# Performance work log

Measured on AMD Instinct MI355X. Metric: run time of the kernel, lower is better.

## Reference

```python
import jax, jax.numpy as jnp
import numpy as np

B, T, V, E, H, L = 128, 512, 128, 256, 1024, 2


def setup_inputs() -> dict:
    key = jax.random.key(0)
    ks = jax.random.split(key, 8)
    scale_e = 1.0 / np.sqrt(E)
    scale0 = 1.0 / np.sqrt(E + H)
    scale1 = 1.0 / np.sqrt(2 * H)
    return {
        "input_batch": jax.random.randint(ks[0], (B, T), 0, V, dtype=jnp.int32),
        "input_lengths": jax.random.randint(ks[1], (B,), 1, T + 1, dtype=jnp.int32),
        "char_embeddings": jax.random.normal(ks[2], (V, E), dtype=jnp.float32) * scale_e,
        "W0": jax.random.normal(ks[3], (E + H, 4 * H), dtype=jnp.float32) * scale0,
        "b0": jnp.zeros((4 * H,), dtype=jnp.float32),
        "W1": jax.random.normal(ks[4], (2 * H, 4 * H), dtype=jnp.float32) * scale1,
        "b1": jnp.zeros((4 * H,), dtype=jnp.float32),
    }


def _lstm_cell(x, h, c, W, b):
    # TF BasicLSTMCell: gates in order (i, j, f, o), forget_bias = 1.0
    z = jnp.concatenate([x, h], axis=-1) @ W + b  # [B, 4H]
    i, j, f, o = jnp.split(z, 4, axis=-1)
    new_c = c * jax.nn.sigmoid(f + 1.0) + jax.nn.sigmoid(i) * jnp.tanh(j)
    new_h = jnp.tanh(new_c) * jax.nn.sigmoid(o)
    return new_h, new_c


def reference(input_batch, input_lengths, char_embeddings, W0, b0, W1, b1):
    # embedding lookup: [B, T, E] -> time-major [T, B, E]
    xs = jnp.swapaxes(char_embeddings[input_batch], 0, 1)
    t_idx = jnp.arange(T, dtype=jnp.int32)
    zeros = jnp.zeros((B, H), dtype=xs.dtype)
    init = (zeros, zeros, zeros, zeros)  # (h0, c0, h1, c1)

    def step(carry, inp):
        h0, c0, h1, c1 = carry
        x_t, t = inp
        mask = (t < input_lengths)[:, None]  # [B, 1] dynamic_rnn length mask
        nh0, nc0 = _lstm_cell(x_t, h0, c0, W0, b0)
        nh0 = jnp.where(mask, nh0, h0)
        nc0 = jnp.where(mask, nc0, c0)
        nh1, nc1 = _lstm_cell(nh0, h1, c1, W1, b1)
        nh1 = jnp.where(mask, nh1, h1)
        nc1 = jnp.where(mask, nc1, c1)
        out = jnp.where(mask, nh1, 0.0)  # dynamic_rnn zeros outputs past length
        return (nh0, nc0, nh1, nc1), out

    _, outputs = jax.lax.scan(step, init, (xs, t_idx))  # outputs: [T, B, H]
    outputs_bt = jnp.swapaxes(outputs, 0, 1)  # [B, T, H]
    # reverse_sequence + slice[:, 0, :] == output at last valid timestep
    idx = (input_lengths - 1)[:, None, None]  # [B, 1, 1]
    encoder_last_output = jnp.take_along_axis(outputs_bt, idx, axis=1)[:, 0, :]
    return encoder_last_output  # [B, H]
```

## Files before the change

### kernel.cpp

```cpp
#include <hip/hip_runtime.h>


namespace {
constexpr int NBLK = 256, THREADS = 512;
constexpr int KT0B = 40;
constexpr int KT1B = 64;
constexpr int NPH = 513;
constexpr int HPS = 128 * 1024;
constexpr int SPIN_CAP = 2000000;
constexpr int F_CREG  = 0;
constexpr int F_BOOT  = 128;
constexpr int F_GARR  = 256;
constexpr int F_XDONE = 768;
constexpr int F_XARR  = 1024;
}

typedef _Float16 f16x8 __attribute__((ext_vector_type(8)));
typedef float f32x4 __attribute__((ext_vector_type(4)));
typedef unsigned u32x4 __attribute__((ext_vector_type(4)));

__host__ __device__ __forceinline__ int fswz(int kk) {
  return ((kk & 15) >> 2) * 8 + (kk >> 4) * 4 + (kk & 3);
}

__device__ __forceinline__ float sigm(float x) { return 1.0f / (1.0f + __expf(-x)); }
__device__ __forceinline__ float tanh_f(float x) {
  float e = __expf(-2.0f * fabsf(x));
  float r = (1.0f - e) / (1.0f + e);
  return x >= 0.0f ? r : -r;
}
__device__ __forceinline__ unsigned short f2h(float f) {
  _Float16 h = (_Float16)f;
  return __builtin_bit_cast(unsigned short, h);
}

__device__ __forceinline__ int load_i32_llc(const int* p) {
  int v;
  asm volatile("global_load_dword %0, %1, off sc0 sc1\n\ts_waitcnt vmcnt(0)"
               : "=v"(v) : "v"(p) : "memory");
  return v;
}
__device__ __forceinline__ uint4 llc_load_issue(const unsigned* p) {
  uint4 v;
  asm volatile("global_load_dwordx4 %0, %1, off sc0 sc1" : "=v"(v) : "v"(p));
  return v;
}
__device__ __forceinline__ void vm_wait0() {
  asm volatile("s_waitcnt vmcnt(0)" ::: "memory");
  __builtin_amdgcn_sched_barrier(0);
}
__device__ __forceinline__ void store_u32_llc(unsigned* p, unsigned v) {
  asm volatile("global_store_dword %0, %1, off sc0 sc1" :: "v"(p), "v"(v) : "memory");
}
__device__ __forceinline__ void store_u16_llc(unsigned short* p, unsigned short v) {
  asm volatile("global_store_short %0, %1, off sc0 sc1" :: "v"(p), "v"(v) : "memory");
}
__device__ __forceinline__ void inv_l1() {
  asm volatile("buffer_inv" ::: "memory");
}
__device__ __forceinline__ int xcc_id() {
  int x;
  asm("s_getreg_b32 %0, hwreg(HW_REG_XCC_ID)" : "=s"(x));
  return x & 7;
}
__device__ __forceinline__ int spin_ge(int* p, int target) {
  for (int it = 0; it < SPIN_CAP; ++it) {
    if (load_i32_llc(p) >= target) return 1;
    __builtin_amdgcn_s_sleep(1);
  }
  return 0;
}
__device__ __forceinline__ f16x8 ash(u32x4 v) { return __builtin_bit_cast(f16x8, v); }
__device__ __forceinline__ f16x8 ash4(uint4 v) { return __builtin_bit_cast(f16x8, v); }

#define MFMA1(acc, ah, bh)                                                    \
  acc = __builtin_amdgcn_mfma_f32_16x16x32_f16(ah, bh, acc, 0, 0, 0);


__global__ void prep_sort(const int* __restrict__ lens, int* __restrict__ perm,
                          int* __restrict__ lenS, int* __restrict__ ncnt) {
  __shared__ int k_[128], p_[128];
  const int tid = threadIdx.x;
  if (tid < 128) { k_[tid] = (lens[tid] << 8) | (127 - tid); p_[tid] = tid; }
  __syncthreads();
  for (int ph = 0; ph < 128; ++ph) {
    if (tid < 64) {
      int a = 2 * tid + (ph & 1), b = a + 1;
      if (b < 128 && k_[a] < k_[b]) {
        int tk = k_[a]; k_[a] = k_[b]; k_[b] = tk;
        int tp = p_[a]; p_[a] = p_[b]; p_[b] = tp;
      }
    }
    __syncthreads();
  }
  if (tid < 128) { perm[tid] = p_[tid]; lenS[tid] = k_[tid] >> 8; }
  if (tid < 512) {
    int c = 0;
    for (int i = 0; i < 128; ++i) c += ((k_[i] >> 8) > tid) ? 1 : 0;
    ncnt[tid] = c;
  }
}

__global__ void prep_emb(const float* __restrict__ emb,
                         unsigned short* __restrict__ ef) {
  int i = blockIdx.x * 256 + threadIdx.x;
  int row = i >> 8, e = i & 255;
  int pos = row * 256 + (e >> 5) * 32 + fswz(e & 31);
  ef[pos] = f2h(emb[i]);
}

__global__ void prep_wslab(const float* __restrict__ W, uint4* __restrict__ Whi,
                           int KT) {
  int e = blockIdx.x * 256 + threadIdx.x;
  int lane = e & 63;
  int kt = (e >> 6) % KT;
  int blk = e / (64 * KT);
  int cf = lane & 15;
  int g = cf & 3, ul = cf >> 2;
  int col = g * 1024 + blk * 4 + ul;
  int kbase = kt * 32 + ((lane >> 4) & 3) * 4;
  unsigned hi[8];
#pragma unroll
  for (int j = 0; j < 8; ++j) {
    int k = kbase + (j & 3) + 16 * (j >> 2);
    float f = W[(size_t)k * 4096 + col];
    hi[j] = __builtin_bit_cast(unsigned short, (_Float16)f);
  }
  uint4 vh;
  vh.x = hi[0] | (hi[1] << 16); vh.y = hi[2] | (hi[3] << 16);
  vh.z = hi[4] | (hi[5] << 16); vh.w = hi[6] | (hi[7] << 16);
  Whi[e] = vh;
}


__global__ __launch_bounds__(THREADS, 1) void lstm_persist(
    const int* __restrict__ ib,
    const float* __restrict__ bias0, const float* __restrict__ bias1,
    const uint4* __restrict__ Whi0g, const uint4* __restrict__ Whi1g,
    const unsigned short* __restrict__ embF,
    const int* __restrict__ perm, const int* __restrict__ lenS,
    const int* __restrict__ ncnt,
    unsigned short* hg0, unsigned short* hg1,
    unsigned short* rep,
    int* ctr, float* __restrict__ out) {
  const int bid = blockIdx.x;
  const int tid = threadIdx.x;
  const int w = tid >> 6;
  const int lane = tid & 63;
  const int lr = lane & 15;
  const int lg4 = ((lane >> 4) & 3) * 4;
  const int slotE = ((lane >> 4) & 3) * 8;
  const int arow = w * 16 + lr;
  const int srow = tid >> 2;
  const int cu = tid & 3;
  const int ug = bid * 4 + cu;
  const int fpos = (ug >> 5) * 32 + fswz(ug & 31);
  const int permA = perm[arow];
  const int cperm = perm[srow];
  const int clen = lenS[srow];

  __shared__ uint4 Wh0[KT0B * 64];
  __shared__ uint4 Wh1[KT1B * 64];
  __shared__ float zb[2][128][17];
  __shared__ int s_x, s_rk, s_R, s_pres, s_ok;

  {
    const uint4* s0 = Whi0g + (size_t)bid * (KT0B * 64);
    for (int i = tid; i < KT0B * 64; i += THREADS) Wh0[i] = s0[i];
    const uint4* s1 = Whi1g + (size_t)bid * (KT1B * 64);
    for (int i = tid; i < KT1B * 64; i += THREADS) Wh1[i] = s1[i];
  }

  float bz0[4], bz1[4];
#pragma unroll
  for (int g = 0; g < 4; ++g) {
    bz0[g] = bias0[g * 1024 + ug];
    bz1[g] = bias1[g * 1024 + ug];
  }
  float c0r = 0.0f, c1r = 0.0f;

  if (tid == 0) {
    s_ok = 1;
    int x = xcc_id();
    s_x = x;
    s_rk = atomicAdd(&ctr[F_CREG + x * 16], 1);
    vm_wait0();
    atomicAdd(&ctr[F_BOOT], 1);
    if (!spin_ge(&ctr[F_BOOT], NBLK)) s_ok = 0;
    int Rv = 1, pres = 0;
    for (int i = 0; i < 8; ++i) {
      int r = load_i32_llc(&ctr[F_CREG + i * 16]);
      if (r > 0) pres |= (1 << i);
      if (i == s_x) Rv = r;
    }
    s_R = Rv;
    s_pres = pres;
  }
  __syncthreads();
  const int xcd = s_x, rk = s_rk, R = s_R, pres = s_pres;
  if (!s_ok) return;

  unsigned short* repB = rep + (size_t)xcd * 2 * HPS;
  const unsigned short* A0 = repB + (size_t)arow * 1024;
  const unsigned short* A1 = repB + HPS + (size_t)arow * 1024;

  const int pl = tid >> 8;
  const int rowoff = (tid >> 7) & 1;
  const int ch = (tid & 127) * 8;
  unsigned short* dp = repB + pl * HPS;

  f32x4 acc0 = (f32x4){0.f, 0.f, 0.f, 0.f};
  if (w * 16 < ncnt[0]) {
    const unsigned short* ef = embF + ib[(size_t)permA * 512] * 256;
#pragma unroll
    for (int kt = 0; kt < 8; ++kt) {
      const f16x8 ah = ash(*(const u32x4*)(ef + kt * 32 + slotE));
      MFMA1(acc0, ah, ash4(Wh0[kt * 64 + lane]))
    }
  }

  for (int p = 0; p < NPH; ++p) {
    const int nact0 = (p < 512) ? ncnt[p] : 0;
    const int nact1 = (p >= 1) ? ncnt[p - 1] : 0;
    const bool doL0 = (p < 512) && (w * 16 < nact0);
    const bool doL1 = (p >= 1) && (w * 16 < nact1);
    const int ncopy = ncnt[p == 0 ? 0 : p - 1];

    f32x4 acc1 = (f32x4){0.f, 0.f, 0.f, 0.f};

    {
      const unsigned short* sp =
          (pl == 0) ? (hg0 + (size_t)((p + 2) % 3) * HPS)
                    : (hg1 + (size_t)((p + 1) % 3) * HPS);
      const int step = 2 * R;
      const int dr0 = 2 * rk + rowoff;
      const int dr1 = dr0 + step, dr2 = dr0 + 2 * step, dr3 = dr0 + 3 * step;
      uint4 dv0, dv1, dv2, dv3;
      if (dr0 < ncopy) dv0 = llc_load_issue((const unsigned*)(sp + dr0 * 1024 + ch));
      if (dr1 < ncopy) dv1 = llc_load_issue((const unsigned*)(sp + dr1 * 1024 + ch));
      if (dr2 < ncopy) dv2 = llc_load_issue((const unsigned*)(sp + dr2 * 1024 + ch));
      if (dr3 < ncopy) dv3 = llc_load_issue((const unsigned*)(sp + dr3 * 1024 + ch));
      vm_wait0();
      if (dr0 < ncopy) *(uint4*)(dp + dr0 * 1024 + ch) = dv0;
      if (dr1 < ncopy) *(uint4*)(dp + dr1 * 1024 + ch) = dv1;
      if (dr2 < ncopy) *(uint4*)(dp + dr2 * 1024 + ch) = dv2;
      if (dr3 < ncopy) *(uint4*)(dp + dr3 * 1024 + ch) = dv3;
      for (int r = dr0 + 4 * step; r < ncopy; r += step) {
        uint4 v = llc_load_issue((const unsigned*)(sp + r * 1024 + ch));
        vm_wait0();
        *(uint4*)(dp + r * 1024 + ch) = v;
      }
    }
    __syncthreads();

    if (tid == 0) store_u32_llc((unsigned*)&ctr[F_XARR + xcd * 64 + rk], p + 1);
    if (tid < 64 && tid < R) {
      if (!spin_ge(&ctr[F_XARR + xcd * 64 + tid], p + 1)) s_ok = 0;
    }
    __syncthreads();
    if (!s_ok) break;
    inv_l1();

    if (doL0 || doL1) {
      u32x4 a[2][8];
#pragma unroll
      for (int i = 0; i < 8; ++i) a[0][i] = *(const u32x4*)(A0 + i * 32 + slotE);
#pragma unroll
      for (int g = 0; g < 4; ++g) {
        const int cb = g & 1;
        if (g < 3) {
#pragma unroll
          for (int i = 0; i < 8; ++i)
            a[cb ^ 1][i] = *(const u32x4*)(A0 + ((g + 1) * 8 + i) * 32 + slotE);
        } else if (doL1) {
#pragma unroll
          for (int i = 0; i < 8; ++i)
            a[cb ^ 1][i] = *(const u32x4*)(A1 + i * 32 + slotE);
        }
#pragma unroll
        for (int i = 0; i < 8; ++i) {
          const int q = g * 8 + i;
          const f16x8 ah = ash(a[cb][i]);
          if (doL0) { MFMA1(acc0, ah, ash4(Wh0[(8 + q) * 64 + lane])) }
          if (doL1) { MFMA1(acc1, ah, ash4(Wh1[q * 64 + lane])) }
        }
      }
      if (doL1) {
#pragma unroll
        for (int g = 0; g < 4; ++g) {
          const int cb = g & 1;
          if (g < 3) {
#pragma unroll
            for (int i = 0; i < 8; ++i)
              a[cb ^ 1][i] = *(const u32x4*)(A1 + ((g + 1) * 8 + i) * 32 + slotE);
          }
#pragma unroll
          for (int i = 0; i < 8; ++i) {
            const int q = g * 8 + i;
            const f16x8 ah = ash(a[cb][i]);
            MFMA1(acc1, ah, ash4(Wh1[(32 + q) * 64 + lane]))
          }
        }
      }
    }

    if (doL0) {
#pragma unroll
      for (int rr = 0; rr < 4; ++rr) zb[0][w * 16 + lg4 + rr][lr] = acc0[rr];
    }
    if (doL1) {
#pragma unroll
      for (int rr = 0; rr < 4; ++rr) zb[1][w * 16 + lg4 + rr][lr] = acc1[rr];
    }
    __syncthreads();
    if (p < 512 && p < clen) {
      const float zi = zb[0][srow][cu * 4 + 0] + bz0[0];
      const float zj = zb[0][srow][cu * 4 + 1] + bz0[1];
      const float zf = zb[0][srow][cu * 4 + 2] + bz0[2];
      const float zo = zb[0][srow][cu * 4 + 3] + bz0[3];
      const float nc = c0r * sigm(zf + 1.0f) + sigm(zi) * tanh_f(zj);
      const float nh = tanh_f(nc) * sigm(zo);
      c0r = nc;
      store_u16_llc(&hg0[(size_t)(p % 3) * HPS + srow * 1024 + fpos], f2h(nh));
    }
    if (p >= 1 && (p - 1) < clen) {
      const float zi = zb[1][srow][cu * 4 + 0] + bz1[0];
      const float zj = zb[1][srow][cu * 4 + 1] + bz1[1];
      const float zf = zb[1][srow][cu * 4 + 2] + bz1[2];
      const float zo = zb[1][srow][cu * 4 + 3] + bz1[3];
      const float nc = c1r * sigm(zf + 1.0f) + sigm(zi) * tanh_f(zj);
      const float nh = tanh_f(nc) * sigm(zo);
      c1r = nc;
      store_u16_llc(&hg1[(size_t)((p + 2) % 3) * HPS + srow * 1024 + fpos], f2h(nh));
      if (p - 1 == clen - 1) out[(size_t)cperm * 1024 + ug] = nh;
    }

    vm_wait0();
    __syncthreads();
    if (tid == 0) store_u32_llc((unsigned*)&ctr[F_GARR + xcd * 64 + rk], p + 1);

    acc0 = (f32x4){0.f, 0.f, 0.f, 0.f};
    if (p + 1 < 512 && (w * 16 < ncnt[p + 1])) {
      const unsigned short* ef = embF + ib[(size_t)permA * 512 + (p + 1)] * 256;
#pragma unroll
      for (int kt = 0; kt < 8; ++kt) {
        const f16x8 ah = ash(*(const u32x4*)(ef + kt * 32 + slotE));
        MFMA1(acc0, ah, ash4(Wh0[kt * 64 + lane]))
      }
    }

    if (rk == 0) {
      if (tid < 64 && tid < R) {
        if (!spin_ge(&ctr[F_GARR + xcd * 64 + tid], p + 1)) s_ok = 0;
      }
      __syncthreads();
      if (tid == 0) store_u32_llc((unsigned*)&ctr[F_XDONE + xcd * 16], p + 1);
    }
    if (tid < 8 && ((pres >> tid) & 1)) {
      if (!spin_ge(&ctr[F_XDONE + tid * 16], p + 1)) s_ok = 0;
    }
    __syncthreads();
    if (!s_ok) break;
  }
}


extern "C" void kernel_launch(void* const* d_in, const int* in_sizes, int n_in,
                              void* d_out, int out_size, void* d_ws, size_t ws_size,
                              hipStream_t stream) {
  const int*   ib   = (const int*)d_in[0];
  const int*   lens = (const int*)d_in[1];
  const float* emb  = (const float*)d_in[2];
  const float* W0   = (const float*)d_in[3];
  const float* b0   = (const float*)d_in[4];
  const float* W1   = (const float*)d_in[5];
  const float* b1   = (const float*)d_in[6];
  (void)in_sizes; (void)n_in; (void)out_size; (void)ws_size;

  char* ws = (char*)d_ws;
  size_t off = 0;
  auto alloc = [&](size_t bytes) { char* q = ws + off; off += (bytes + 255) & ~(size_t)255; return q; };

  int*            ctr  = (int*)alloc(8192);
  unsigned short* hg0  = (unsigned short*)alloc((size_t)3 * HPS * 2);
  unsigned short* hg1  = (unsigned short*)alloc((size_t)3 * HPS * 2);
  const size_t zero_bytes = off;
  unsigned short* embF = (unsigned short*)alloc(128 * 256 * 2);
  int*            perm = (int*)alloc(4096);
  int*            lenS = perm + 128;
  int*            ncnt = perm + 256;
  unsigned short* rep  = (unsigned short*)alloc((size_t)8 * 2 * HPS * 2);
  uint4*          Whi0 = (uint4*)alloc((size_t)NBLK * KT0B * 64 * 16);
  uint4*          Whi1 = (uint4*)alloc((size_t)NBLK * KT1B * 64 * 16);

  hipMemsetAsync(d_ws, 0, zero_bytes, stream);
  prep_sort<<<1, 512, 0, stream>>>(lens, perm, lenS, ncnt);
  prep_emb<<<128, 256, 0, stream>>>(emb, embF);
  prep_wslab<<<(NBLK * KT0B * 64) / 256, 256, 0, stream>>>(W0, Whi0, KT0B);
  prep_wslab<<<(NBLK * KT1B * 64) / 256, 256, 0, stream>>>(W1, Whi1, KT1B);
  lstm_persist<<<NBLK, THREADS, 0, stream>>>(
      ib, b0, b1, Whi0, Whi1, embF,
      perm, lenS, ncnt, hg0, hg1, rep, ctr, (float*)d_out);
}
```

Baseline: 7.470 ms.

## Drop per-XCD hidden-state replication; read shared double-buffered state after L2 invalidate

Removes the per-step copy of the hidden states from global triple buffers into per-XCD replicas, along with the extra intra-XCD barrier that guarded it. Blocks now write h directly into a single global double-buffered array and, after the global step barrier, invalidate L2 and L1 so the next step's MFMA operand loads fetch fresh data. This cuts a full copy pass and one barrier per timestep. In exchange, every block's operand reads miss its local L2 and go to memory or the last-level cache, and the output store is now written through with sc0 sc1.

```diff
diff --git a/kernel.cpp b/kernel.cpp
--- a/kernel.cpp
+++ b/kernel.cpp
@@ -12,7 +12,6 @@
 constexpr int F_BOOT  = 128;
 constexpr int F_GARR  = 256;
 constexpr int F_XDONE = 768;
-constexpr int F_XARR  = 1024;
 }
 
 typedef _Float16 f16x8 __attribute__((ext_vector_type(8)));
@@ -40,11 +39,6 @@
                : "=v"(v) : "v"(p) : "memory");
   return v;
 }
-__device__ __forceinline__ uint4 llc_load_issue(const unsigned* p) {
-  uint4 v;
-  asm volatile("global_load_dwordx4 %0, %1, off sc0 sc1" : "=v"(v) : "v"(p));
-  return v;
-}
 __device__ __forceinline__ void vm_wait0() {
   asm volatile("s_waitcnt vmcnt(0)" ::: "memory");
   __builtin_amdgcn_sched_barrier(0);
@@ -55,7 +49,11 @@
 __device__ __forceinline__ void store_u16_llc(unsigned short* p, unsigned short v) {
   asm volatile("global_store_short %0, %1, off sc0 sc1" :: "v"(p), "v"(v) : "memory");
 }
-__device__ __forceinline__ void inv_l1() {
+__device__ __forceinline__ void store_f32_llc(float* p, float v) {
+  asm volatile("global_store_dword %0, %1, off sc0 sc1" :: "v"(p), "v"(v) : "memory");
+}
+__device__ __forceinline__ void inv_l2_l1() {
+  asm volatile("buffer_inv sc1" ::: "memory");
   asm volatile("buffer_inv" ::: "memory");
 }
 __device__ __forceinline__ int xcc_id() {
@@ -140,7 +138,6 @@
     const unsigned short* __restrict__ embF,
     const int* __restrict__ perm, const int* __restrict__ lenS,
     const int* __restrict__ ncnt,
-    unsigned short* hg0, unsigned short* hg1,
     unsigned short* rep,
     int* ctr, float* __restrict__ out) {
   const int bid = blockIdx.x;
@@ -200,15 +197,6 @@
   const int xcd = s_x, rk = s_rk, R = s_R, pres = s_pres;
   if (!s_ok) return;
 
-  unsigned short* repB = rep + (size_t)xcd * 2 * HPS;
-  const unsigned short* A0 = repB + (size_t)arow * 1024;
-  const unsigned short* A1 = repB + HPS + (size_t)arow * 1024;
-
-  const int pl = tid >> 8;
-  const int rowoff = (tid >> 7) & 1;
-  const int ch = (tid & 127) * 8;
-  unsigned short* dp = repB + pl * HPS;
-
   f32x4 acc0 = (f32x4){0.f, 0.f, 0.f, 0.f};
   if (w * 16 < ncnt[0]) {
     const unsigned short* ef = embF + ib[(size_t)permA * 512] * 256;
@@ -224,42 +212,13 @@
     const int nact1 = (p >= 1) ? ncnt[p - 1] : 0;
     const bool doL0 = (p < 512) && (w * 16 < nact0);
     const bool doL1 = (p >= 1) && (w * 16 < nact1);
-    const int ncopy = ncnt[p == 0 ? 0 : p - 1];
 
     f32x4 acc1 = (f32x4){0.f, 0.f, 0.f, 0.f};
 
-    {
-      const unsigned short* sp =
-          (pl == 0) ? (hg0 + (size_t)((p + 2) % 3) * HPS)
-                    : (hg1 + (size_t)((p + 1) % 3) * HPS);
-      const int step = 2 * R;
-      const int dr0 = 2 * rk + rowoff;
-      const int dr1 = dr0 + step, dr2 = dr0 + 2 * step, dr3 = dr0 + 3 * step;
-      uint4 dv0, dv1, dv2, dv3;
-      if (dr0 < ncopy) dv0 = llc_load_issue((const unsigned*)(sp + dr0 * 1024 + ch));
-      if (dr1 < ncopy) dv1 = llc_load_issue((const unsigned*)(sp + dr1 * 1024 + ch));
-      if (dr2 < ncopy) dv2 = llc_load_issue((const unsigned*)(sp + dr2 * 1024 + ch));
-      if (dr3 < ncopy) dv3 = llc_load_issue((const unsigned*)(sp + dr3 * 1024 + ch));
-      vm_wait0();
-      if (dr0 < ncopy) *(uint4*)(dp + dr0 * 1024 + ch) = dv0;
-      if (dr1 < ncopy) *(uint4*)(dp + dr1 * 1024 + ch) = dv1;
-      if (dr2 < ncopy) *(uint4*)(dp + dr2 * 1024 + ch) = dv2;
-      if (dr3 < ncopy) *(uint4*)(dp + dr3 * 1024 + ch) = dv3;
-      for (int r = dr0 + 4 * step; r < ncopy; r += step) {
-        uint4 v = llc_load_issue((const unsigned*)(sp + r * 1024 + ch));
-        vm_wait0();
-        *(uint4*)(dp + r * 1024 + ch) = v;
-      }
-    }
-    __syncthreads();
-
-    if (tid == 0) store_u32_llc((unsigned*)&ctr[F_XARR + xcd * 64 + rk], p + 1);
-    if (tid < 64 && tid < R) {
-      if (!spin_ge(&ctr[F_XARR + xcd * 64 + tid], p + 1)) s_ok = 0;
-    }
-    __syncthreads();
-    if (!s_ok) break;
-    inv_l1();
+    const unsigned short* A0 = rep + (size_t)((p & 1) * 2 + 0) * HPS + (size_t)arow * 1024;
+    const unsigned short* A1 = rep + (size_t)((p & 1) * 2 + 1) * HPS + (size_t)arow * 1024;
+    unsigned short* w0p = rep + (size_t)(((p + 1) & 1) * 2 + 0) * HPS;
+    unsigned short* w1p = rep + (size_t)(((p + 1) & 1) * 2 + 1) * HPS;
 
     if (doL0 || doL1) {
       u32x4 a[2][8];
@@ -321,7 +280,7 @@
       const float nc = c0r * sigm(zf + 1.0f) + sigm(zi) * tanh_f(zj);
       const float nh = tanh_f(nc) * sigm(zo);
       c0r = nc;
-      store_u16_llc(&hg0[(size_t)(p % 3) * HPS + srow * 1024 + fpos], f2h(nh));
+      store_u16_llc(&w0p[(size_t)srow * 1024 + fpos], f2h(nh));
     }
     if (p >= 1 && (p - 1) < clen) {
       const float zi = zb[1][srow][cu * 4 + 0] + bz1[0];
@@ -331,8 +290,8 @@
       const float nc = c1r * sigm(zf + 1.0f) + sigm(zi) * tanh_f(zj);
       const float nh = tanh_f(nc) * sigm(zo);
       c1r = nc;
-      store_u16_llc(&hg1[(size_t)((p + 2) % 3) * HPS + srow * 1024 + fpos], f2h(nh));
-      if (p - 1 == clen - 1) out[(size_t)cperm * 1024 + ug] = nh;
+      store_u16_llc(&w1p[(size_t)srow * 1024 + fpos], f2h(nh));
+      if (p - 1 == clen - 1) store_f32_llc(&out[(size_t)cperm * 1024 + ug], nh);
     }
 
     vm_wait0();
@@ -361,6 +320,7 @@
     }
     __syncthreads();
     if (!s_ok) break;
+    inv_l2_l1();
   }
 }
 
@@ -382,14 +342,12 @@
   auto alloc = [&](size_t bytes) { char* q = ws + off; off += (bytes + 255) & ~(size_t)255; return q; };
 
   int*            ctr  = (int*)alloc(8192);
-  unsigned short* hg0  = (unsigned short*)alloc((size_t)3 * HPS * 2);
-  unsigned short* hg1  = (unsigned short*)alloc((size_t)3 * HPS * 2);
+  unsigned short* rep  = (unsigned short*)alloc((size_t)2 * 2 * HPS * 2);
   const size_t zero_bytes = off;
   unsigned short* embF = (unsigned short*)alloc(128 * 256 * 2);
   int*            perm = (int*)alloc(4096);
   int*            lenS = perm + 128;
   int*            ncnt = perm + 256;
-  unsigned short* rep  = (unsigned short*)alloc((size_t)8 * 2 * HPS * 2);
   uint4*          Whi0 = (uint4*)alloc((size_t)NBLK * KT0B * 64 * 16);
   uint4*          Whi1 = (uint4*)alloc((size_t)NBLK * KT1B * 64 * 16);
 
@@ -400,5 +358,5 @@
   prep_wslab<<<(NBLK * KT1B * 64) / 256, 256, 0, stream>>>(W1, Whi1, KT1B);
   lstm_persist<<<NBLK, THREADS, 0, stream>>>(
       ib, b0, b1, Whi0, Whi1, embF,
-      perm, lenS, ncnt, hg0, hg1, rep, ctr, (float*)d_out);
-}
+      perm, lenS, ncnt, rep, ctr, (float*)d_out);
+}
```

Result: slower. 13.71 ms (+83.5%).
